# Kernel tuning notes

Hardware: AMD Instinct MI355X
Metric: run time of the kernel (lower is better)

The kernel has to match this reference:

```python
import jax, jax.numpy as jnp
import numpy as np

D_MODEL = 2048
N_HEADS = 32
N_KV_HEADS = 8
ROPE_BASE = 10000.0


def setup_inputs() -> dict:
    key = jax.random.key(0)
    ks = jax.random.split(key, 5)
    b, s, d = 2, 2048, D_MODEL
    hd = d // N_HEADS
    scale = 0.02
    return {
        "x": jax.random.normal(ks[0], (b, s, d), jnp.float32),
        "wq": jax.random.normal(ks[1], (N_HEADS * hd, d), jnp.float32) * scale,
        "wk": jax.random.normal(ks[2], (N_KV_HEADS * hd, d), jnp.float32) * scale,
        "wv": jax.random.normal(ks[3], (N_KV_HEADS * hd, d), jnp.float32) * scale,
        "wo": jax.random.normal(ks[4], (d, N_HEADS * hd), jnp.float32) * scale,
    }


def _rope_cos_sin(seq_len, head_dim):
    # theta_j = base^(-2j/d); freqs[i, j] = i * theta_j; repeat-interleave x2 on last dim
    theta = 1.0 / (ROPE_BASE ** (jnp.arange(0, head_dim, 2, dtype=jnp.float32) / head_dim))
    freqs = jnp.arange(seq_len, dtype=jnp.float32)[:, None] * theta[None, :]  # [S, hd/2]
    cos = jnp.repeat(jnp.cos(freqs), 2, axis=-1)[None, :, None, :]  # [1, S, 1, hd]
    sin = jnp.repeat(jnp.sin(freqs), 2, axis=-1)[None, :, None, :]
    return cos, sin


def _rotate(t):
    # interleaved rotate-half: (x0, x1, x2, x3, ...) -> (-x1, x0, -x3, x2, ...)
    t1 = t[..., ::2]
    t2 = t[..., 1::2]
    return jnp.stack([-t2, t1], axis=-1).reshape(t.shape)


def reference(x, wq, wk, wv, wo):
    b, s, d = x.shape
    hd = d // N_HEADS
    n_rep = N_HEADS // N_KV_HEADS

    q = (x @ wq.T).reshape(b, s, N_HEADS, hd)       # [b, s, H, hd]
    k = (x @ wk.T).reshape(b, s, N_KV_HEADS, hd)    # [b, s, G, hd]
    v = (x @ wv.T).reshape(b, s, N_KV_HEADS, hd)

    cos, sin = _rope_cos_sin(s, hd)
    q = q * cos + _rotate(q) * sin
    k = k * cos + _rotate(k) * sin

    # GQA without physical KV replication: group query heads by shared KV head.
    # repeat_interleave(n_rep, dim=2) maps kv head g -> query heads [g*n_rep, (g+1)*n_rep)
    qg = q.reshape(b, s, N_KV_HEADS, n_rep, hd)
    scale = 1.0 / jnp.sqrt(jnp.asarray(hd, q.dtype))
    scores = jnp.einsum('bqgrd,bkgd->bgrqk', qg, k) * scale  # [b, G, rep, Sq, Sk]

    causal = jnp.tril(jnp.ones((s, s), dtype=bool))
    scores = jnp.where(causal[None, None, None], scores, jnp.asarray(-jnp.inf, scores.dtype))
    attn = jax.nn.softmax(scores, axis=-1)

    out = jnp.einsum('bgrqk,bkgd->bqgrd', attn, v).reshape(b, s, N_HEADS * hd)
    return out @ wo.T
```

## Files before the change

### kernel.cpp

```cpp
#include <hip/hip_runtime.h>

typedef unsigned short u16;
typedef __attribute__((ext_vector_type(8))) short bf16x8;
typedef __attribute__((ext_vector_type(4))) float f32x4;

#define LOG2E 1.44269504088896340736f

__device__ inline u16 f2b(float f) {
    unsigned int u = __builtin_bit_cast(unsigned int, f);
    unsigned int r = u + 0x7fffu + ((u >> 16) & 1u);
    return (u16)(r >> 16);
}
__device__ inline float b2f(u16 h) {
    unsigned int u = ((unsigned int)h) << 16;
    return __builtin_bit_cast(float, u);
}

#define GLOAD_LDS16(g, l) \
    __builtin_amdgcn_global_load_lds( \
        (const __attribute__((address_space(1))) unsigned int*)(g), \
        (__attribute__((address_space(3))) unsigned int*)(l), 16, 0, 0)

__global__ __launch_bounds__(256) void cast_all(
    const float* __restrict__ x, const float* __restrict__ wq,
    const float* __restrict__ wk, const float* __restrict__ wv,
    const float* __restrict__ wo, u16* __restrict__ xb,
    u16* __restrict__ wqkvb, u16* __restrict__ wob) {
    long i = ((long)blockIdx.x * 256 + threadIdx.x) * 8;
    const float* s;
    u16* d;
    if (i < 8388608)       { s = x  + i;              d = xb + i; }
    else if (i < 12582912) { s = wq + (i - 8388608);  d = wqkvb + (i - 8388608); }
    else if (i < 13631488) { s = wk + (i - 12582912); d = wqkvb + 4194304 + (i - 12582912); }
    else if (i < 14680064) { s = wv + (i - 13631488); d = wqkvb + 5242880 + (i - 13631488); }
    else                   { s = wo + (i - 14680064); d = wob + (i - 14680064); }
    float4 v0 = *(const float4*)s;
    float4 v1 = *(const float4*)(s + 4);
    ushort4 o0 = make_ushort4(f2b(v0.x), f2b(v0.y), f2b(v0.z), f2b(v0.w));
    ushort4 o1 = make_ushort4(f2b(v1.x), f2b(v1.y), f2b(v1.z), f2b(v1.w));
    *(ushort4*)d = o0;
    *(ushort4*)(d + 4) = o1;
}

__global__ __launch_bounds__(256) void rope_vtrans(
    u16* __restrict__ qkv, u16* __restrict__ VT, float qscale) {
    const int S = 2048, RS = 3072;
    int tid = threadIdx.x;
    if (blockIdx.x < 5120) {
        int idx = blockIdx.x * 256 + tid;
        int row = idx / 320;
        int rem = idx - row * 320;
        int head = rem >> 3, chunk = rem & 7;
        int pos = row & 2047;
        int coloff;
        float scale;
        if (head < 32) { coloff = head * 64;               scale = qscale; }
        else           { coloff = 2048 + (head - 32) * 64; scale = 1.0f; }
        u16* p = qkv + (size_t)row * RS + coloff + chunk * 8;
        bf16x8 v = *(bf16x8*)p;
        float t0 = exp2f((float)(chunk * 4) * -0.41524101186092f);
        const float tc[4] = {1.0f, 0.74989420933246f, 0.56234132519035f, 0.42169650342858f};
        float fpos = (float)pos;
        #pragma unroll
        for (int i = 0; i < 4; i++) {
            float f = fpos * (t0 * tc[i]);
            float rev = f * 0.15915494309189535f;
            rev = rev - floorf(rev);
            float sn = __builtin_amdgcn_sinf(rev);
            float cs = __builtin_amdgcn_cosf(rev);
            float e0 = b2f((u16)v[2 * i]), e1 = b2f((u16)v[2 * i + 1]);
            v[2 * i]     = (short)f2b((e0 * cs - e1 * sn) * scale);
            v[2 * i + 1] = (short)f2b((e1 * cs + e0 * sn) * scale);
        }
        *(bf16x8*)p = v;
    } else {
        int bid = blockIdx.x - 5120;
        int st = bid & 31, g = (bid >> 5) & 7, b = bid >> 8;
        __shared__ u16 T[64 * 72];
        for (int c = tid; c < 512; c += 256) {
            int sr = c >> 3, dc = (c & 7) * 8;
            *(bf16x8*)&T[sr * 72 + dc] =
                *(const bf16x8*)(qkv + ((size_t)b * S + st * 64 + sr) * RS + 2560 + g * 64 + dc);
        }
        __syncthreads();
        for (int c = tid; c < 512; c += 256) {
            int d = c >> 3, sc = (c & 7) * 8;
            bf16x8 o;
            #pragma unroll
            for (int j = 0; j < 8; j++) o[j] = (short)T[(sc + j) * 72 + d];
            *(bf16x8*)(VT + ((size_t)((b * 8 + g) * 64 + d)) * S + st * 64 + sc) = o;
        }
    }
}

#define MMAQ(MH, NH, AR, BR) do { \
    __builtin_amdgcn_s_setprio(1); \
    _Pragma("unroll") \
    for (int m2 = 0; m2 < 4; m2++) { \
        _Pragma("unroll") \
        for (int n2 = 0; n2 < 2; n2++) { \
            acc[(MH)*4+m2][(NH)*2+n2] = __builtin_amdgcn_mfma_f32_16x16x32_bf16( \
                AR[m2][0], BR[n2][0], acc[(MH)*4+m2][(NH)*2+n2], 0, 0, 0); \
            acc[(MH)*4+m2][(NH)*2+n2] = __builtin_amdgcn_mfma_f32_16x16x32_bf16( \
                AR[m2][1], BR[n2][1], acc[(MH)*4+m2][(NH)*2+n2], 0, 0, 0); \
        } \
    } \
    __builtin_amdgcn_s_setprio(0); \
} while (0)

#define BAR()    do { __builtin_amdgcn_s_barrier(); \
                      __builtin_amdgcn_sched_barrier(0); } while (0)
#define LGKM0()  do { asm volatile("s_waitcnt lgkmcnt(0)" ::: "memory"); \
                      __builtin_amdgcn_sched_barrier(0); } while (0)
#define VMCNT(n) do { asm volatile("s_waitcnt vmcnt(" #n ")" ::: "memory"); \
                      __builtin_amdgcn_sched_barrier(0); } while (0)

__global__ __launch_bounds__(512) void gemm_bt256(
    const u16* __restrict__ A, const u16* __restrict__ B, void* __restrict__ Cv,
    int M, int N, int K, int c_is_f32) {
    __shared__ u16 As[32768];
    __shared__ u16 Bs[32768];
    const int tid = threadIdx.x;
    const int w = tid >> 6, lane = tid & 63;
    const int ln = lane & 15, quad = lane >> 4;
    const int wr = w >> 2, wc = w & 3;

    const int gx = gridDim.x;
    const int nwg = gx * gridDim.y;
    const int bid = blockIdx.y * gx + blockIdx.x;
    const int cpx = nwg >> 3;
    const int swz = (bid & 7) * cpx + (bid >> 3);
    const int m0 = (swz / gx) * 256, n0 = (swz % gx) * 256;

    const int l3 = lane >> 3, l7 = lane & 7;
    const u16* Ast = A + (size_t)(m0 + w * 8 + l3) * K + (l7 ^ l3) * 8;
    const u16* Bst = B + (size_t)(n0 + w * 8 + l3) * K + (l7 ^ l3) * 8;

    auto stageA = [&](int u, int h) {
        const u16* g = Ast + (size_t)(h * 128) * K + u * 64;
        u16* d = As + ((u & 1) * 2 + h) * 8192 + w * 512;
        GLOAD_LDS16(g, d);
        GLOAD_LDS16(g + (size_t)64 * K, d + 4096);
    };
    auto stageB = [&](int u, int h) {
        const u16* g = Bst + (size_t)(h * 128) * K + u * 64;
        u16* d = Bs + ((u & 1) * 2 + h) * 8192 + w * 512;
        GLOAD_LDS16(g, d);
        GLOAD_LDS16(g + (size_t)64 * K, d + 4096);
    };

    const int xs0 = ((quad) ^ (ln & 7)) * 8;
    const int xs1 = ((4 + quad) ^ (ln & 7)) * 8;

    bf16x8 a[4][2], b0[2][2], b1[2][2];
    auto loadA = [&](int u, int mh, bf16x8 (&dst)[4][2]) {
        const u16* base = As + ((u & 1) * 2 + wr) * 8192 + (mh * 64 + ln) * 64;
        #pragma unroll
        for (int m2 = 0; m2 < 4; m2++) {
            dst[m2][0] = *(const bf16x8*)(base + m2 * 1024 + xs0);
            dst[m2][1] = *(const bf16x8*)(base + m2 * 1024 + xs1);
        }
    };
    auto loadB = [&](int u, int nh, bf16x8 (&dst)[2][2]) {
        const u16* base = Bs + ((u & 1) * 2 + (wc >> 1)) * 8192
                        + ((wc & 1) * 64 + nh * 32 + ln) * 64;
        #pragma unroll
        for (int n2 = 0; n2 < 2; n2++) {
            dst[n2][0] = *(const bf16x8*)(base + n2 * 1024 + xs0);
            dst[n2][1] = *(const bf16x8*)(base + n2 * 1024 + xs1);
        }
    };

    f32x4 acc[8][4] = {};
    const int NT = K >> 6;

    stageB(0, 0); stageB(0, 1);
    stageA(0, 0); stageA(0, 1);
    stageB(1, 0); stageB(1, 1);
    VMCNT(4);
    BAR();

    for (int u = 0; u < NT; ++u) {
        loadA(u, 0, a);
        loadB(u, 0, b0);
        if (u + 1 < NT) stageA(u + 1, 0);
        BAR(); LGKM0();
        MMAQ(0, 0, a, b0);
        BAR();
        loadB(u, 1, b1);
        if (u + 1 < NT) stageA(u + 1, 1);
        BAR(); LGKM0();
        MMAQ(0, 1, a, b1);
        BAR();
        loadA(u, 1, a);
        if (u + 2 < NT) stageB(u + 2, 0);
        BAR(); LGKM0();
        MMAQ(1, 1, a, b1);
        BAR();
        if (u + 2 < NT) stageB(u + 2, 1);
        BAR();
        MMAQ(1, 0, a, b0);
        if (u + 2 < NT)      { VMCNT(4); }
        else if (u + 1 < NT) { VMCNT(0); }
        BAR();
    }

    #pragma unroll
    for (int mi = 0; mi < 8; mi++)
        #pragma unroll
        for (int ni = 0; ni < 4; ni++)
            #pragma unroll
            for (int r = 0; r < 4; r++) {
                int row = m0 + wr * 128 + mi * 16 + quad * 4 + r;
                int col = n0 + wc * 64 + ni * 16 + ln;
                float v = acc[mi][ni][r];
                if (c_is_f32) ((float*)Cv)[(size_t)row * N + col] = v;
                else          ((u16*)Cv)[(size_t)row * N + col] = f2b(v);
            }
}

__global__ __launch_bounds__(512) void attn_kernel(
    const u16* __restrict__ QKV, const u16* __restrict__ VT, u16* __restrict__ O) {
    const int S = 2048, RS = 3072, DO = 2048;
    const int bid = blockIdx.x;
    const int swz = (bid & 7) * 64 + (bid >> 3);
    const int p = swz & 15, hp = (swz >> 4) & 15, b = swz >> 8;
    const int g = hp >> 1;
    const int qtl = p, qth = 31 - p;
    const int tid = threadIdx.x;
    const int lane = tid & 63, wave = tid >> 6;
    const int hw = wave >> 2, lw = wave & 3;
    const int h = hp * 2 + hw;
    const int ln = lane & 15, quad = lane >> 4;

    __shared__ u16 Ks[2][64 * 64];
    __shared__ u16 Ps[4][64 * 68];
    u16* Psh = &Ps[hw * 2 + 0][0];
    u16* Psl = &Ps[hw * 2 + 1][0];

    const u16* Qb = QKV + (size_t)b * S * RS + h * 64 + quad * 8;
    bf16x8 aqh0 = *(const bf16x8*)(Qb + (size_t)(qth * 64 + lw * 16 + ln) * RS);
    bf16x8 aqh1 = *(const bf16x8*)(Qb + (size_t)(qth * 64 + lw * 16 + ln) * RS + 32);
    bf16x8 aql0 = *(const bf16x8*)(Qb + (size_t)(qtl * 64 + lw * 16 + ln) * RS);
    bf16x8 aql1 = *(const bf16x8*)(Qb + (size_t)(qtl * 64 + lw * 16 + ln) * RS + 32);

    const u16* Kb = QKV + (size_t)b * S * RS + 2048 + g * 64;
    const u16* VTb = VT + (size_t)(b * 8 + g) * 64 * S;

    const bf16x8 vones = {0x3F80, 0x3F80, 0x3F80, 0x3F80, 0x3F80, 0x3F80, 0x3F80, 0x3F80};

    f32x4 acch[5] = {}, accl[5] = {};

    const int kr = tid >> 3;
    const int ks = tid & 7;
    const int kswz = ((ks ^ (kr & 7)) * 8);
    bf16x8 kreg;
    bf16x8 vr[2][4];
    auto loadK = [&](int kt) {
        kreg = *(const bf16x8*)(Kb + (size_t)(kt * 64 + kr) * RS + ks * 8);
    };
    auto loadV = [&](int kt) {
        #pragma unroll
        for (int kk = 0; kk < 2; kk++)
            #pragma unroll
            for (int nt = 0; nt < 4; nt++)
                vr[kk][nt] = *(const bf16x8*)(VTb + (size_t)(nt * 16 + ln) * S
                                              + kt * 64 + kk * 32 + quad * 8);
    };

    auto body = [&](int kt, bool DUAL, bool MH, bool ML) {
        u16* KsC = &Ks[kt & 1][0];
        u16* KsN = &Ks[(kt & 1) ^ 1][0];
        if (kt < qth) {
            *(bf16x8*)&KsN[kr * 64 + kswz] = kreg;
        }
        if (kt + 2 <= qth) loadK(kt + 2);

        const int rsw = ln & 7;
        f32x4 sh[4] = {}, sl[4] = {};
        __builtin_amdgcn_s_setprio(1);
        #pragma unroll
        for (int nt = 0; nt < 4; nt++) {
            bf16x8 bk0 = *(const bf16x8*)&KsC[(nt * 16 + ln) * 64 + ((quad ^ rsw) * 8)];
            bf16x8 bk1 = *(const bf16x8*)&KsC[(nt * 16 + ln) * 64 + (((quad + 4) ^ rsw) * 8)];
            sh[nt] = __builtin_amdgcn_mfma_f32_16x16x32_bf16(aqh0, bk0, sh[nt], 0, 0, 0);
            sh[nt] = __builtin_amdgcn_mfma_f32_16x16x32_bf16(aqh1, bk1, sh[nt], 0, 0, 0);
            if (DUAL) {
                sl[nt] = __builtin_amdgcn_mfma_f32_16x16x32_bf16(aql0, bk0, sl[nt], 0, 0, 0);
                sl[nt] = __builtin_amdgcn_mfma_f32_16x16x32_bf16(aql1, bk1, sl[nt], 0, 0, 0);
            }
        }
        __builtin_amdgcn_s_setprio(0);

        if (MH) {
            #pragma unroll
            for (int nt = 0; nt < 4; nt++)
                #pragma unroll
                for (int r = 0; r < 4; r++)
                    if (nt * 16 + ln > lw * 16 + quad * 4 + r) sh[nt][r] = -INFINITY;
        }
        #pragma unroll
        for (int nt = 0; nt < 4; nt++)
            #pragma unroll
            for (int r = 0; r < 4; r++) {
                float pv = exp2f(sh[nt][r]);
                Psh[(lw * 16 + quad * 4 + r) * 68 + nt * 16 + ln] =
                    (u16)(__builtin_bit_cast(unsigned int, pv) >> 16);
            }
        if (DUAL) {
            if (ML) {
                #pragma unroll
                for (int nt = 0; nt < 4; nt++)
                    #pragma unroll
                    for (int r = 0; r < 4; r++)
                        if (nt * 16 + ln > lw * 16 + quad * 4 + r) sl[nt][r] = -INFINITY;
            }
            #pragma unroll
            for (int nt = 0; nt < 4; nt++)
                #pragma unroll
                for (int r = 0; r < 4; r++) {
                    float pv = exp2f(sl[nt][r]);
                    Psl[(lw * 16 + quad * 4 + r) * 68 + nt * 16 + ln] =
                        (u16)(__builtin_bit_cast(unsigned int, pv) >> 16);
                }
        }

        __builtin_amdgcn_s_setprio(1);
        #pragma unroll
        for (int kk = 0; kk < 2; kk++) {
            bf16x8 aph = *(const bf16x8*)&Psh[(lw * 16 + ln) * 68 + kk * 32 + quad * 8];
            #pragma unroll
            for (int nt = 0; nt < 4; nt++)
                acch[nt] = __builtin_amdgcn_mfma_f32_16x16x32_bf16(aph, vr[kk][nt], acch[nt], 0, 0, 0);
            acch[4] = __builtin_amdgcn_mfma_f32_16x16x32_bf16(aph, vones, acch[4], 0, 0, 0);
            if (DUAL) {
                bf16x8 apl = *(const bf16x8*)&Psl[(lw * 16 + ln) * 68 + kk * 32 + quad * 8];
                #pragma unroll
                for (int nt = 0; nt < 4; nt++)
                    accl[nt] = __builtin_amdgcn_mfma_f32_16x16x32_bf16(apl, vr[kk][nt], accl[nt], 0, 0, 0);
                accl[4] = __builtin_amdgcn_mfma_f32_16x16x32_bf16(apl, vones, accl[4], 0, 0, 0);
            }
        }
        __builtin_amdgcn_s_setprio(0);

        if (kt < qth) loadV(kt + 1);
        __syncthreads();
    };

    loadK(0);
    loadV(0);
    *(bf16x8*)&Ks[0][kr * 64 + kswz] = kreg;
    loadK(1);
    __syncthreads();

    for (int kt = 0; kt < qtl; kt++) body(kt, true, false, false);
    body(qtl, true, false, true);
    for (int kt = qtl + 1; kt < qth; kt++) body(kt, false, false, false);
    body(qth, false, true, false);

    u16* Ob = O + (size_t)b * S * DO + h * 64;
    #pragma unroll
    for (int r = 0; r < 4; r++) {
        float invh = 1.0f / acch[4][r];
        float invl = 1.0f / accl[4][r];
        int qh = qth * 64 + lw * 16 + quad * 4 + r;
        int ql = qtl * 64 + lw * 16 + quad * 4 + r;
        #pragma unroll
        for (int nt = 0; nt < 4; nt++) {
            Ob[(size_t)qh * DO + nt * 16 + ln] = f2b(acch[nt][r] * invh);
            Ob[(size_t)ql * DO + nt * 16 + ln] = f2b(accl[nt][r] * invl);
        }
    }
}

extern "C" void kernel_launch(void* const* d_in, const int* in_sizes, int n_in,
                              void* d_out, int out_size, void* d_ws, size_t ws_size,
                              hipStream_t stream) {
    const float* x  = (const float*)d_in[0];
    const float* wq = (const float*)d_in[1];
    const float* wk = (const float*)d_in[2];
    const float* wv = (const float*)d_in[3];
    const float* wo = (const float*)d_in[4];

    const int B = 2, S = 2048, D = 2048;
    const int M = B * S;
    const int NQKV = 3072;

    char* ws = (char*)d_ws;
    size_t off = 0;
    auto alloc = [&](size_t bytes) {
        void* p = ws + off;
        off += (bytes + 255) & ~(size_t)255;
        return p;
    };
    u16* xb    = (u16*)alloc((size_t)M * D * 2);
    u16* wqkvb = (u16*)alloc((size_t)NQKV * D * 2);
    u16* wob   = (u16*)alloc((size_t)D * D * 2);
    u16* QKV   = (u16*)alloc((size_t)M * NQKV * 2);
    u16* AO = xb;
    u16* VT = wqkvb;

    cast_all<<<dim3(9216), 256, 0, stream>>>(x, wq, wk, wv, wo, xb, wqkvb, wob);

    gemm_bt256<<<dim3(NQKV / 256, M / 256), 512, 0, stream>>>(xb, wqkvb, QKV, M, NQKV, D, 0);

    const float sscale = 0.125f * LOG2E;
    rope_vtrans<<<dim3(5632), 256, 0, stream>>>(QKV, VT, sscale);

    attn_kernel<<<dim3(512), 512, 0, stream>>>(QKV, VT, AO);

    gemm_bt256<<<dim3(D / 256, M / 256), 512, 0, stream>>>(AO, wob, d_out, M, D, D, 1);
}
```

Before: 365.9 us.

## Stage V tiles through double-buffered LDS instead of per-wave global register loads

```diff
diff --git a/kernel.cpp b/kernel.cpp
--- a/kernel.cpp
+++ b/kernel.cpp
@@ -234,6 +234,7 @@
     const int ln = lane & 15, quad = lane >> 4;
 
     __shared__ u16 Ks[2][64 * 64];
+    __shared__ u16 Vs[2][64 * 64];
     __shared__ u16 Ps[4][64 * 68];
     u16* Psh = &Ps[hw * 2 + 0][0];
     u16* Psl = &Ps[hw * 2 + 1][0];
@@ -254,27 +255,22 @@
     const int kr = tid >> 3;
     const int ks = tid & 7;
     const int kswz = ((ks ^ (kr & 7)) * 8);
-    bf16x8 kreg;
-    bf16x8 vr[2][4];
-    auto loadK = [&](int kt) {
+    bf16x8 kreg, vreg;
+    auto loadKV = [&](int kt) {
         kreg = *(const bf16x8*)(Kb + (size_t)(kt * 64 + kr) * RS + ks * 8);
-    };
-    auto loadV = [&](int kt) {
-        #pragma unroll
-        for (int kk = 0; kk < 2; kk++)
-            #pragma unroll
-            for (int nt = 0; nt < 4; nt++)
-                vr[kk][nt] = *(const bf16x8*)(VTb + (size_t)(nt * 16 + ln) * S
-                                              + kt * 64 + kk * 32 + quad * 8);
+        vreg = *(const bf16x8*)(VTb + (size_t)kr * S + kt * 64 + ks * 8);
     };
 
     auto body = [&](int kt, bool DUAL, bool MH, bool ML) {
         u16* KsC = &Ks[kt & 1][0];
-        u16* KsN = &Ks[(kt & 1) ^ 1][0];
+        u16* VsC = &Vs[kt & 1][0];
         if (kt < qth) {
+            u16* KsN = &Ks[(kt & 1) ^ 1][0];
+            u16* VsN = &Vs[(kt & 1) ^ 1][0];
             *(bf16x8*)&KsN[kr * 64 + kswz] = kreg;
-        }
-        if (kt + 2 <= qth) loadK(kt + 2);
+            *(bf16x8*)&VsN[kr * 64 + kswz] = vreg;
+        }
+        if (kt + 2 <= qth) loadKV(kt + 2);
 
         const int rsw = ln & 7;
         f32x4 sh[4] = {}, sl[4] = {};
@@ -329,28 +325,29 @@
         #pragma unroll
         for (int kk = 0; kk < 2; kk++) {
             bf16x8 aph = *(const bf16x8*)&Psh[(lw * 16 + ln) * 68 + kk * 32 + quad * 8];
-            #pragma unroll
-            for (int nt = 0; nt < 4; nt++)
-                acch[nt] = __builtin_amdgcn_mfma_f32_16x16x32_bf16(aph, vr[kk][nt], acch[nt], 0, 0, 0);
+            bf16x8 apl;
+            if (DUAL) apl = *(const bf16x8*)&Psl[(lw * 16 + ln) * 68 + kk * 32 + quad * 8];
+            #pragma unroll
+            for (int nt = 0; nt < 4; nt++) {
+                bf16x8 bv = *(const bf16x8*)&VsC[(nt * 16 + ln) * 64
+                                                 + (((kk * 4 + quad) ^ rsw) * 8)];
+                acch[nt] = __builtin_amdgcn_mfma_f32_16x16x32_bf16(aph, bv, acch[nt], 0, 0, 0);
+                if (DUAL)
+                    accl[nt] = __builtin_amdgcn_mfma_f32_16x16x32_bf16(apl, bv, accl[nt], 0, 0, 0);
+            }
             acch[4] = __builtin_amdgcn_mfma_f32_16x16x32_bf16(aph, vones, acch[4], 0, 0, 0);
-            if (DUAL) {
-                bf16x8 apl = *(const bf16x8*)&Psl[(lw * 16 + ln) * 68 + kk * 32 + quad * 8];
-                #pragma unroll
-                for (int nt = 0; nt < 4; nt++)
-                    accl[nt] = __builtin_amdgcn_mfma_f32_16x16x32_bf16(apl, vr[kk][nt], accl[nt], 0, 0, 0);
+            if (DUAL)
                 accl[4] = __builtin_amdgcn_mfma_f32_16x16x32_bf16(apl, vones, accl[4], 0, 0, 0);
-            }
         }
         __builtin_amdgcn_s_setprio(0);
 
-        if (kt < qth) loadV(kt + 1);
         __syncthreads();
     };
 
-    loadK(0);
-    loadV(0);
+    loadKV(0);
     *(bf16x8*)&Ks[0][kr * 64 + kswz] = kreg;
-    loadK(1);
+    *(bf16x8*)&Vs[0][kr * 64 + kswz] = vreg;
+    loadKV(1);
     __syncthreads();
 
     for (int kt = 0; kt < qtl; kt++) body(kt, true, false, false);
```

After: 336.3 us. 8.1% less time.
